# Kernel optimization log

Hardware: AMD Instinct MI355X
Metric: run time of the kernel (lower is better)

Reference implementation:

```python
import jax, jax.numpy as jnp
import numpy as np

EPS = 1e-12  # F.normalize eps


def qweight(r, i, j, k):
    # Hamilton-product block matrix: (out, in, kh, kw) from 4 blocks of (out//4, in//4, kh, kw)
    row_r = jnp.concatenate([r, -i, -j, -k], axis=1)
    row_i = jnp.concatenate([i, r, -k, j], axis=1)
    row_j = jnp.concatenate([j, k, r, -i], axis=1)
    row_k = jnp.concatenate([k, -j, i, r], axis=1)
    return jnp.concatenate([row_r, row_i, row_j, row_k], axis=0)


def qconv(x, r, i, j, k, b, stride, pad):
    w = qweight(r, i, j, k)
    y = jax.lax.conv_general_dilated(
        x, w, window_strides=(stride, stride),
        padding=[(pad, pad), (pad, pad)],
        dimension_numbers=('NCHW', 'OIHW', 'NCHW'))
    return y + b[None, :, None, None]


def setup_inputs() -> dict:
    key = jax.random.key(0)
    ks = jax.random.split(key, 16)
    dim, heads, B, H, W = 128, 4, 2, 128, 128
    d4 = dim // 4
    std = 0.02
    inp = {
        'x': jax.random.normal(ks[0], (B, dim, H, W), jnp.float32),
        'qkv_r': jax.random.normal(ks[1], (3 * d4, d4, 1, 1), jnp.float32) * std,
        'qkv_i': jax.random.normal(ks[2], (3 * d4, d4, 1, 1), jnp.float32) * std,
        'qkv_j': jax.random.normal(ks[3], (3 * d4, d4, 1, 1), jnp.float32) * std,
        'qkv_k': jax.random.normal(ks[4], (3 * d4, d4, 1, 1), jnp.float32) * std,
        'qkv_b': jnp.zeros((3 * dim,), jnp.float32),
        'dw_r': jax.random.normal(ks[5], (3 * d4, 3 * d4, 3, 3), jnp.float32) * std,
        'dw_i': jax.random.normal(ks[6], (3 * d4, 3 * d4, 3, 3), jnp.float32) * std,
        'dw_j': jax.random.normal(ks[7], (3 * d4, 3 * d4, 3, 3), jnp.float32) * std,
        'dw_k': jax.random.normal(ks[8], (3 * d4, 3 * d4, 3, 3), jnp.float32) * std,
        'dw_b': jnp.zeros((3 * dim,), jnp.float32),
        'po_r': jax.random.normal(ks[9], (d4, d4, 1, 1), jnp.float32) * std,
        'po_i': jax.random.normal(ks[10], (d4, d4, 1, 1), jnp.float32) * std,
        'po_j': jax.random.normal(ks[11], (d4, d4, 1, 1), jnp.float32) * std,
        'po_k': jax.random.normal(ks[12], (d4, d4, 1, 1), jnp.float32) * std,
        'po_b': jnp.zeros((dim,), jnp.float32),
        'temperature': jnp.ones((heads, 1, 1), jnp.float32),
    }
    return inp


def reference(x, qkv_r, qkv_i, qkv_j, qkv_k, qkv_b,
              dw_r, dw_i, dw_j, dw_k, dw_b,
              po_r, po_i, po_j, po_k, po_b, temperature):
    b, c, h, w = x.shape
    heads = temperature.shape[0]
    ch = c // heads  # channels per head

    qkv = qconv(x, qkv_r, qkv_i, qkv_j, qkv_k, qkv_b, 1, 0)
    qkv = qconv(qkv, dw_r, dw_i, dw_j, dw_k, dw_b, 1, 1)
    q, k, v = jnp.split(qkv, 3, axis=1)

    def to_heads(t):  # b (head c) h w -> b head c (h w)
        return t.reshape(b, heads, ch, h * w)

    q, k, v = to_heads(q), to_heads(k), to_heads(v)
    # L2-normalize along spatial axis (torch F.normalize semantics)
    q = q / jnp.maximum(jnp.linalg.norm(q, axis=-1, keepdims=True), EPS)
    k = k / jnp.maximum(jnp.linalg.norm(k, axis=-1, keepdims=True), EPS)

    attn = jnp.einsum('bhcs,bhds->bhcd', q, k) * temperature[None]
    attn = jax.nn.softmax(attn, axis=-1)
    out = jnp.einsum('bhcd,bhds->bhcs', attn, v)

    out = out.reshape(b, c, h, w)
    out = qconv(out, po_r, po_i, po_j, po_k, po_b, 1, 0)
    return out
```

## Files before the change

kernel.cpp:

```cpp
#include <hip/hip_runtime.h>
#include <hip/hip_bf16.h>
#include <string.h>

typedef __hip_bfloat16 bf16;
typedef __bf16 bf16x8 __attribute__((ext_vector_type(8)));
typedef float f32x4 __attribute__((ext_vector_type(4)));

typedef __attribute__((address_space(1))) void* gas_ptr;
typedef __attribute__((address_space(3))) void* las_ptr;

__device__ __forceinline__ void gload_lds16(const void* g, void* l) {
  __builtin_amdgcn_global_load_lds((gas_ptr)(void*)g, (las_ptr)l, 16, 0, 0);
}


__device__ __forceinline__ void qexpand(const float* r, const float* i_, const float* j_,
                                        const float* k_, bf16* dst, int O4, int I4, int taps,
                                        int gid) {
  int C = 4 * I4;
  int o   = gid / (taps * C);
  int rem = gid % (taps * C);
  int tap = rem / C, c = rem % C;
  int br = o / O4, orr = o % O4, bc = c / I4, ic = c % I4;
  const float* srcs[4] = { r, i_, j_, k_ };
  const int   comp[4][4] = { {0,1,2,3}, {1,0,3,2}, {2,3,0,1}, {3,2,1,0} };
  const float sgn [4][4] = { {1,-1,-1,-1}, {1,1,-1,1}, {1,1,1,-1}, {1,-1,1,1} };
  float v = srcs[comp[br][bc]][(size_t)(orr * I4 + ic) * taps + tap];
  dst[gid] = __float2bfloat16(v * sgn[br][bc]);
}

#define N_W1 49152
#define N_W2 1327104
#define N_W3 16384
#define N_BR 396288
#define N_MI 900
#define N_SQ 512
#define N_SR 8192
#define N_PREP (N_W1 + N_W2 + N_W3 + N_BR + N_MI + N_SQ + N_SR)

__global__ void prep(const float* __restrict__ qr, const float* __restrict__ qi,
                     const float* __restrict__ qj, const float* __restrict__ qk,
                     const float* __restrict__ dr, const float* __restrict__ di,
                     const float* __restrict__ dj, const float* __restrict__ dk,
                     const float* __restrict__ pr, const float* __restrict__ pi,
                     const float* __restrict__ pj, const float* __restrict__ pk,
                     const float* __restrict__ qb, const float* __restrict__ db,
                     const float* __restrict__ pb, const float* __restrict__ tp,
                     bf16* __restrict__ W1t, bf16* __restrict__ W2t, bf16* __restrict__ W3t,
                     bf16* __restrict__ q1p, float* __restrict__ misc,
                     float* __restrict__ ssq, float* __restrict__ Sraw) {
  int gid = blockIdx.x * 256 + threadIdx.x;
  if (gid < N_W1) { qexpand(qr, qi, qj, qk, W1t, 96, 32, 1, gid); return; }
  gid -= N_W1;
  if (gid < N_W2) { qexpand(dr, di, dj, dk, W2t, 96, 96, 9, gid); return; }
  gid -= N_W2;
  if (gid < N_W3) { qexpand(pr, pi, pj, pk, W3t, 32, 32, 1, gid); return; }
  gid -= N_W3;
  if (gid < N_BR) {
    int b = gid / (516 * 384);
    int rem = gid % (516 * 384);
    int cell = rem / 384, c = rem % 384;
    int hp, wp;
    if      (cell < 130) { hp = 0;   wp = cell; }
    else if (cell < 260) { hp = 129; wp = cell - 130; }
    else if (cell < 388) { hp = cell - 260 + 1; wp = 0; }
    else                 { hp = cell - 388 + 1; wp = 129; }
    q1p[((size_t)((b * 130 + hp) * 130) + wp) * 384 + c] = __float2bfloat16(0.0f);
    return;
  }
  gid -= N_BR;
  if (gid < N_MI) {
    if (gid < 384)      misc[gid] = qb[gid];
    else if (gid < 768) misc[gid] = db[gid - 384];
    else if (gid < 896) misc[gid] = pb[gid - 768];
    else                misc[gid] = tp[gid - 896];
    return;
  }
  gid -= N_MI;
  if (gid < N_SQ) { ssq[gid] = 0.0f; return; }
  gid -= N_SQ;
  if (gid < N_SR) { Sraw[gid] = 0.0f; return; }
}

__global__ __launch_bounds__(256) void gemm_qkv1f(const float* __restrict__ x,
                                                  const bf16* __restrict__ wt,
                                                  const float* __restrict__ bias,
                                                  bf16* __restrict__ out) {
  __shared__ __align__(16) bf16 Axl[4 * 64 * 32];
  __shared__ __align__(16) bf16 Bl [4 * 128 * 32];
  const int h = blockIdx.x, wh = blockIdx.y, b = blockIdx.z;
  const int tid = threadIdx.x, wid = tid >> 6, lane = tid & 63;
  const int l16 = lane & 15, q = lane >> 4;
  const int wm = (wid & 1) * 32, wn = (wid >> 1) * 64;
  {
    const int c = tid >> 1, seg = tid & 1;
    const float* src = x + ((size_t)(b * 128 + c) << 14) + h * 128 + wh * 64 + seg * 32;
    bf16* dstc = Axl + (c >> 5) * 2048 + (c & 31);
    for (int j = 0; j < 8; ++j) {
      float4 v = *(const float4*)(src + j * 4);
      int w0 = seg * 32 + j * 4;
      dstc[(w0 + 0) * 32] = __float2bfloat16(v.x);
      dstc[(w0 + 1) * 32] = __float2bfloat16(v.y);
      dstc[(w0 + 2) * 32] = __float2bfloat16(v.z);
      dstc[(w0 + 3) * 32] = __float2bfloat16(v.w);
    }
  }
  for (int ot = 0; ot < 3; ++ot) {
    __syncthreads();
    const bf16* bbase = wt + (size_t)ot * 16384;
    for (int i = 0; i < 8; ++i) {
      int ci = wid * 512 + i * 64 + lane;
      int chunk = ci >> 9, rem = ci & 511;
      int o = rem >> 2, part = rem & 3;
      gload_lds16(bbase + o * 128 + chunk * 32 + part * 8, Bl + (size_t)(wid * 512 + i * 64) * 8);
    }
    __syncthreads();
    f32x4 acc[2][4] = {};
    for (int k = 0; k < 4; ++k) {
      bf16x8 af[2], bfr[4];
      for (int mi = 0; mi < 2; ++mi)
        af[mi] = *(const bf16x8*)&Axl[k * 2048 + (wm + mi * 16 + l16) * 32 + q * 8];
      for (int ni = 0; ni < 4; ++ni)
        bfr[ni] = *(const bf16x8*)&Bl[k * 4096 + (wn + ni * 16 + l16) * 32 + q * 8];
      for (int mi = 0; mi < 2; ++mi)
        for (int ni = 0; ni < 4; ++ni)
          acc[mi][ni] = __builtin_amdgcn_mfma_f32_16x16x32_bf16(af[mi], bfr[ni], acc[mi][ni], 0, 0, 0);
    }
    for (int ni = 0; ni < 4; ++ni) {
      int o = ot * 128 + wn + ni * 16 + l16;
      float bv = bias[o];
      for (int mi = 0; mi < 2; ++mi) {
        int w0 = wh * 64 + wm + mi * 16 + q * 4;
        for (int r = 0; r < 4; ++r) {
          int w = w0 + r;
          size_t idx = ((size_t)((b * 130 + h + 1) * 130) + (w + 1)) * 384 + o;
          out[idx] = __float2bfloat16(acc[mi][ni][r] + bv);
        }
      }
    }
    __syncthreads();
  }
}

__global__ __launch_bounds__(256, 2) void conv3x3(const bf16* __restrict__ in,
                                                  const bf16* __restrict__ wt,
                                                  const float* __restrict__ bias,
                                                  bf16* __restrict__ out) {
  __shared__ __align__(16) short Al[6 * 132 * 32];
  __shared__ __align__(16) short Bl[9 * 48 * 32];
  const int lid = blockIdx.x;
  const int xcd = lid & 7, slot = lid >> 3;
  const int b = xcd & 1;
  const int h0 = (xcd >> 1) * 32 + (slot & 7) * 4;
  const int ob = (slot >> 3) * 48;
  const int tid = threadIdx.x, wid = tid >> 6, lane = tid & 63;
  const int l16 = lane & 15, q = lane >> 4;
  f32x4 acc[8][3] = {};
  const bf16* abase = in + (size_t)b * 130 * 130 * 384;
  const bf16* bbase = wt + (size_t)ob * 3456;
  for (int c0 = 0; c0 < 384; c0 += 32) {
    __syncthreads();
    for (int i = 0; i < 12; ++i) {
      int g = wid * 792 + i * 64;
      int ci = g + lane;
      int row = ci / 528, rem = ci % 528;
      int w = rem >> 2, part = rem & 3;
      gload_lds16(abase + ((size_t)(h0 + row) * 130 + w) * 384 + c0 + part * 8, &Al[g * 8]);
    }
    if (lane < 24) {
      int g = wid * 792 + 768;
      int ci = g + lane;
      int row = ci / 528, rem = ci % 528;
      int w = rem >> 2, part = rem & 3;
      gload_lds16(abase + ((size_t)(h0 + row) * 130 + w) * 384 + c0 + part * 8, &Al[g * 8]);
    }
    for (int i = 0; i < 6; ++i) {
      int g = wid * 432 + i * 64;
      int ci = g + lane;
      int tap = ci / 192, rem = ci % 192;
      int o = rem >> 2, part = rem & 3;
      gload_lds16(bbase + (size_t)o * 3456 + tap * 384 + c0 + part * 8, &Bl[g * 8]);
    }
    if (lane < 48) {
      int g = wid * 432 + 384;
      int ci = g + lane;
      int tap = ci / 192, rem = ci % 192;
      int o = rem >> 2, part = rem & 3;
      gload_lds16(bbase + (size_t)o * 3456 + tap * 384 + c0 + part * 8, &Bl[g * 8]);
    }
    __syncthreads();
    for (int dh = 0; dh < 3; ++dh)
      for (int dw = 0; dw < 3; ++dw) {
        bf16x8 af[8], bfr[3];
        for (int mi = 0; mi < 8; ++mi)
          af[mi] = *(const bf16x8*)&Al[((wid + dh) * 132 + mi * 16 + l16 + dw) * 32 + q * 8];
        for (int ni = 0; ni < 3; ++ni)
          bfr[ni] = *(const bf16x8*)&Bl[((dh * 3 + dw) * 48 + ni * 16 + l16) * 32 + q * 8];
        for (int mi = 0; mi < 8; ++mi)
          for (int ni = 0; ni < 3; ++ni)
            acc[mi][ni] = __builtin_amdgcn_mfma_f32_16x16x32_bf16(af[mi], bfr[ni], acc[mi][ni], 0, 0, 0);
      }
  }
  const int h = h0 + wid;
  for (int ni = 0; ni < 3; ++ni) {
    int o = ob + ni * 16 + l16;
    float bv = bias[o];
    for (int mi = 0; mi < 8; ++mi) {
      int w0 = mi * 16 + q * 4;
      for (int r = 0; r < 4; ++r) {
        int w = w0 + r;
        out[((size_t)(b * 16384 + h * 128 + w)) * 384 + o] = __float2bfloat16(acc[mi][ni][r] + bv);
      }
    }
  }
}

__global__ __launch_bounds__(256) void attn_qk(const bf16* __restrict__ q2,
                                               float* __restrict__ Sraw,
                                               float* __restrict__ ssq) {
  const int sc = blockIdx.x, h = blockIdx.y, b = blockIdx.z;
  const int t = threadIdx.x;
  __shared__ bf16 qt[64][32];
  __shared__ bf16 kt[64][32];
  __shared__ float Sl[1024];
  __shared__ float nql[32], nkl[32];
  for (int i = t; i < 1024; i += 256) Sl[i] = 0.0f;
  if (t < 32) nql[t] = 0.0f;
  else if (t < 64) nkl[t - 32] = 0.0f;
  const int slq = t >> 2, seg = t & 3;
  const int slot = t & 63, sg = t >> 6;
  const int cg = (slot & 7) * 4, dg = (slot >> 3) * 4;
  float acc[4][4] = {};
  float sq[4] = {}, sk[4] = {};
  for (int it = 0; it < 8; ++it) {
    int sbase = sc * 512 + it * 64;
    __syncthreads();
    {
      size_t rq = ((size_t)(b * 16384 + sbase + slq)) * 384 + h * 32 + seg * 8;
      *(bf16x8*)&qt[slq][seg * 8] = *(const bf16x8*)&q2[rq];
      *(bf16x8*)&kt[slq][seg * 8] = *(const bf16x8*)&q2[rq + 128];
    }
    __syncthreads();
    for (int sl = sg * 16; sl < sg * 16 + 16; ++sl) {
      float qv[4], kv[4];
      for (int a = 0; a < 4; ++a) qv[a] = __bfloat162float(qt[sl][cg + a]);
      for (int d = 0; d < 4; ++d) kv[d] = __bfloat162float(kt[sl][dg + d]);
      if (dg == 0) for (int a = 0; a < 4; ++a) sq[a] += qv[a] * qv[a];
      if (cg == 0) for (int d = 0; d < 4; ++d) sk[d] += kv[d] * kv[d];
      for (int a = 0; a < 4; ++a)
        for (int d = 0; d < 4; ++d) acc[a][d] += qv[a] * kv[d];
    }
  }
  for (int a = 0; a < 4; ++a)
    for (int d = 0; d < 4; ++d)
      atomicAdd(&Sl[(cg + a) * 32 + dg + d], acc[a][d]);
  if (dg == 0) for (int a = 0; a < 4; ++a) atomicAdd(&nql[cg + a], sq[a]);
  if (cg == 0) for (int d = 0; d < 4; ++d) atomicAdd(&nkl[dg + d], sk[d]);
  __syncthreads();
  float* Sg = Sraw + (size_t)((b * 4 + h) * 1024);
  for (int i = t * 4; i < t * 4 + 4; ++i) atomicAdd(&Sg[i], Sl[i]);
  if (t < 32) atomicAdd(&ssq[b * 256 + h * 32 + t], nql[t]);
  else if (t < 64) atomicAdd(&ssq[b * 256 + 128 + h * 32 + (t - 32)], nkl[t - 32]);
}

__global__ __launch_bounds__(256) void attn_out(const bf16* __restrict__ q2,
                                                const float* __restrict__ Sraw,
                                                const float* __restrict__ ssq,
                                                const float* __restrict__ misc,
                                                const bf16* __restrict__ w3,
                                                float* __restrict__ out) {
  __shared__ __align__(16) bf16 Ml[4 * 128 * 32];
  __shared__ float Pl[4][32][32];
  __shared__ __align__(16) short Bl[128 * 32];
  __shared__ float rqa[128], rka[128];
  const int tile = blockIdx.x;
  const int b = tile >> 7, s0 = (tile & 127) * 128;
  const int t = threadIdx.x;
  const int wid = t >> 6, lane = t & 63;
  const int l16 = lane & 15, q = lane >> 4;
  {
    float v = ssq[b * 256 + t];
    float rv = 1.0f / fmaxf(sqrtf(fmaxf(v, 0.0f)), 1e-12f);
    if (t < 128) rqa[t] = rv; else rka[t - 128] = rv;
  }
  __syncthreads();
  if (t < 128) {
    int hh = t >> 5, c = t & 31;
    const float* Sr = Sraw + ((size_t)((b * 4 + hh) * 32 + c)) * 32;
    float tv = misc[896 + hh];
    float rq = rqa[t];
    float row[32];
    float m = -1e30f;
    for (int d = 0; d < 32; ++d) { row[d] = Sr[d] * tv * rq * rka[hh * 32 + d]; m = fmaxf(m, row[d]); }
    float sum = 0.0f;
    for (int d = 0; d < 32; ++d) { row[d] = expf(row[d] - m); sum += row[d]; }
    float inv = 1.0f / sum;
    for (int d = 0; d < 32; ++d) Pl[hh][c][d] = row[d] * inv;
  }
  __syncthreads();
  {
    const int o = t >> 1, half = t & 1;
    for (int hh2 = 0; hh2 < 2; ++hh2) {
      int hv = half * 2 + hh2;
      float w3r[32];
      const bf16* wrow = w3 + o * 128 + hv * 32;
      for (int c = 0; c < 32; ++c) w3r[c] = __bfloat162float(wrow[c]);
      for (int d = 0; d < 32; ++d) {
        float s = 0.0f;
        for (int c = 0; c < 32; ++c) s += w3r[c] * Pl[hv][c][d];
        Ml[hv * 4096 + o * 32 + d] = __float2bfloat16(s);
      }
    }
  }
  f32x4 acc[4][4] = {};
  const int wmo = (wid & 1) * 64, wns = (wid >> 1) * 64;
  for (int kc = 0; kc < 4; ++kc) {
    __syncthreads();
    for (int i = 0; i < 2; ++i) {
      int ci = i * 256 + t;
      int s = ci >> 2, part = ci & 3;
      gload_lds16(q2 + ((size_t)(b * 16384 + s0 + s)) * 384 + 256 + kc * 32 + part * 8,
                  &Bl[(size_t)(i * 256 + wid * 64) * 8]);
    }
    __syncthreads();
    bf16x8 af[4], bfr[4];
    for (int mi = 0; mi < 4; ++mi)
      af[mi] = *(const bf16x8*)&Ml[kc * 4096 + (wmo + mi * 16 + l16) * 32 + q * 8];
    for (int ni = 0; ni < 4; ++ni)
      bfr[ni] = *(const bf16x8*)&Bl[(wns + ni * 16 + l16) * 32 + q * 8];
    for (int mi = 0; mi < 4; ++mi)
      for (int ni = 0; ni < 4; ++ni)
        acc[mi][ni] = __builtin_amdgcn_mfma_f32_16x16x32_bf16(af[mi], bfr[ni], acc[mi][ni], 0, 0, 0);
  }
  for (int ni = 0; ni < 4; ++ni) {
    int s = s0 + wns + ni * 16 + l16;
    for (int mi = 0; mi < 4; ++mi) {
      int o0 = wmo + mi * 16 + q * 4;
      for (int r = 0; r < 4; ++r) {
        int o = o0 + r;
        out[(size_t)b * 2097152 + (size_t)o * 16384 + s] = acc[mi][ni][r] + misc[768 + o];
      }
    }
  }
}

extern "C" void kernel_launch(void* const* d_in, const int* in_sizes, int n_in,
                              void* d_out, int out_size, void* d_ws, size_t ws_size,
                              hipStream_t stream) {
  const float* x     = (const float*)d_in[0];
  const float* qkv_r = (const float*)d_in[1];
  const float* qkv_i = (const float*)d_in[2];
  const float* qkv_j = (const float*)d_in[3];
  const float* qkv_k = (const float*)d_in[4];
  const float* qkv_b = (const float*)d_in[5];
  const float* dw_r  = (const float*)d_in[6];
  const float* dw_i  = (const float*)d_in[7];
  const float* dw_j  = (const float*)d_in[8];
  const float* dw_k  = (const float*)d_in[9];
  const float* dw_b  = (const float*)d_in[10];
  const float* po_r  = (const float*)d_in[11];
  const float* po_i  = (const float*)d_in[12];
  const float* po_j  = (const float*)d_in[13];
  const float* po_k  = (const float*)d_in[14];
  const float* po_b  = (const float*)d_in[15];
  const float* temp  = (const float*)d_in[16];

  char* ws = (char*)d_ws;
  size_t off = 0;
  auto alloc = [&](size_t bytes) { char* p = ws + off; off += (bytes + 255) & ~(size_t)255; return p; };
  bf16* q1p  = (bf16*)alloc((size_t)2 * 130 * 130 * 384 * 2);
  bf16* q2   = (bf16*)alloc((size_t)2 * 16384 * 384 * 2);
  bf16* W1t  = (bf16*)alloc((size_t)384 * 128 * 2);
  bf16* W2t  = (bf16*)alloc((size_t)384 * 3456 * 2);
  bf16* W3t  = (bf16*)alloc((size_t)128 * 128 * 2);
  float* ssq  = (float*)alloc((size_t)2 * 256 * 4);
  float* Sraw = (float*)alloc((size_t)2 * 4 * 32 * 32 * 4);
  float* misc = (float*)alloc((size_t)900 * 4);

  prep<<<(N_PREP + 255) / 256, 256, 0, stream>>>(qkv_r, qkv_i, qkv_j, qkv_k,
                                                 dw_r, dw_i, dw_j, dw_k,
                                                 po_r, po_i, po_j, po_k,
                                                 qkv_b, dw_b, po_b, temp,
                                                 W1t, W2t, W3t, q1p, misc, ssq, Sraw);
  gemm_qkv1f<<<dim3(128, 2, 2), 256, 0, stream>>>(x, W1t, misc, q1p);
  conv3x3<<<512, 256, 0, stream>>>(q1p, W2t, misc + 384, q2);
  attn_qk<<<dim3(32, 4, 2), 256, 0, stream>>>(q2, Sraw, ssq);
  attn_out<<<256, 256, 0, stream>>>(q2, Sraw, ssq, misc, W3t, (float*)d_out);
}
```

Before: 229.5 us.

## Fuse prep into QKV GEMM and merge attention kernels with counter sync

The weight-expansion/prep kernel is merged into the first pointwise QKV GEMM. The W1 quaternion weight is now expanded directly into LDS inside the GEMM blocks, while the remaining blocks do the other prep work. The two attention kernels become one launch: the first 256 blocks compute the Gram matrix and norms, then bump a global counter, and the output blocks spin on that counter before the softmax and projection. This removes two launches and their inter-kernel gaps. The cost is redundant W1 expansion per block and a spin-wait that relies on producer blocks being scheduled first.

```diff
diff --git a/kernel.cpp b/kernel.cpp
--- a/kernel.cpp
+++ b/kernel.cpp
@@ -29,67 +29,70 @@
   dst[gid] = __float2bfloat16(v * sgn[br][bc]);
 }
 
-#define N_W1 49152
 #define N_W2 1327104
 #define N_W3 16384
 #define N_BR 396288
 #define N_MI 900
 #define N_SQ 512
 #define N_SR 8192
-#define N_PREP (N_W1 + N_W2 + N_W3 + N_BR + N_MI + N_SQ + N_SR)
-
-__global__ void prep(const float* __restrict__ qr, const float* __restrict__ qi,
-                     const float* __restrict__ qj, const float* __restrict__ qk,
-                     const float* __restrict__ dr, const float* __restrict__ di,
-                     const float* __restrict__ dj, const float* __restrict__ dk,
-                     const float* __restrict__ pr, const float* __restrict__ pi,
-                     const float* __restrict__ pj, const float* __restrict__ pk,
-                     const float* __restrict__ qb, const float* __restrict__ db,
-                     const float* __restrict__ pb, const float* __restrict__ tp,
-                     bf16* __restrict__ W1t, bf16* __restrict__ W2t, bf16* __restrict__ W3t,
-                     bf16* __restrict__ q1p, float* __restrict__ misc,
-                     float* __restrict__ ssq, float* __restrict__ Sraw) {
-  int gid = blockIdx.x * 256 + threadIdx.x;
-  if (gid < N_W1) { qexpand(qr, qi, qj, qk, W1t, 96, 32, 1, gid); return; }
-  gid -= N_W1;
-  if (gid < N_W2) { qexpand(dr, di, dj, dk, W2t, 96, 96, 9, gid); return; }
-  gid -= N_W2;
-  if (gid < N_W3) { qexpand(pr, pi, pj, pk, W3t, 32, 32, 1, gid); return; }
-  gid -= N_W3;
-  if (gid < N_BR) {
-    int b = gid / (516 * 384);
-    int rem = gid % (516 * 384);
-    int cell = rem / 384, c = rem % 384;
-    int hp, wp;
-    if      (cell < 130) { hp = 0;   wp = cell; }
-    else if (cell < 260) { hp = 129; wp = cell - 130; }
-    else if (cell < 388) { hp = cell - 260 + 1; wp = 0; }
-    else                 { hp = cell - 388 + 1; wp = 129; }
-    q1p[((size_t)((b * 130 + hp) * 130) + wp) * 384 + c] = __float2bfloat16(0.0f);
+#define N_CT 64
+#define N_PREP (N_W2 + N_W3 + N_BR + N_MI + N_SQ + N_SR + N_CT)
+#define PREP_BLOCKS ((N_PREP + 255) / 256)
+
+__global__ __launch_bounds__(256) void qkv1f_prep(
+    const float* __restrict__ x,
+    const float* __restrict__ qr, const float* __restrict__ qi,
+    const float* __restrict__ qj, const float* __restrict__ qk,
+    const float* __restrict__ qkv_b,
+    const float* __restrict__ dr, const float* __restrict__ di,
+    const float* __restrict__ dj, const float* __restrict__ dk,
+    const float* __restrict__ pr, const float* __restrict__ pi,
+    const float* __restrict__ pj, const float* __restrict__ pk,
+    const float* __restrict__ qb, const float* __restrict__ db,
+    const float* __restrict__ pb, const float* __restrict__ tp,
+    bf16* __restrict__ W2t, bf16* __restrict__ W3t,
+    bf16* __restrict__ q1p, float* __restrict__ misc,
+    float* __restrict__ ssq, float* __restrict__ Sraw, int* __restrict__ ctr) {
+  const int lid = blockIdx.x;
+  const int tid = threadIdx.x;
+  if (lid >= 512) {
+    int gid = (lid - 512) * 256 + tid;
+    if (gid < N_W2) { qexpand(dr, di, dj, dk, W2t, 96, 96, 9, gid); return; }
+    gid -= N_W2;
+    if (gid < N_W3) { qexpand(pr, pi, pj, pk, W3t, 32, 32, 1, gid); return; }
+    gid -= N_W3;
+    if (gid < N_BR) {
+      int b = gid / (516 * 384);
+      int rem = gid % (516 * 384);
+      int cell = rem / 384, c = rem % 384;
+      int hp, wp;
+      if      (cell < 130) { hp = 0;   wp = cell; }
+      else if (cell < 260) { hp = 129; wp = cell - 130; }
+      else if (cell < 388) { hp = cell - 260 + 1; wp = 0; }
+      else                 { hp = cell - 388 + 1; wp = 129; }
+      q1p[((size_t)((b * 130 + hp) * 130) + wp) * 384 + c] = __float2bfloat16(0.0f);
+      return;
+    }
+    gid -= N_BR;
+    if (gid < N_MI) {
+      if (gid < 384)      misc[gid] = qb[gid];
+      else if (gid < 768) misc[gid] = db[gid - 384];
+      else if (gid < 896) misc[gid] = pb[gid - 768];
+      else                misc[gid] = tp[gid - 896];
+      return;
+    }
+    gid -= N_MI;
+    if (gid < N_SQ) { ssq[gid] = 0.0f; return; }
+    gid -= N_SQ;
+    if (gid < N_SR) { Sraw[gid] = 0.0f; return; }
+    gid -= N_SR;
+    if (gid < N_CT) { ctr[gid] = 0; return; }
     return;
   }
-  gid -= N_BR;
-  if (gid < N_MI) {
-    if (gid < 384)      misc[gid] = qb[gid];
-    else if (gid < 768) misc[gid] = db[gid - 384];
-    else if (gid < 896) misc[gid] = pb[gid - 768];
-    else                misc[gid] = tp[gid - 896];
-    return;
-  }
-  gid -= N_MI;
-  if (gid < N_SQ) { ssq[gid] = 0.0f; return; }
-  gid -= N_SQ;
-  if (gid < N_SR) { Sraw[gid] = 0.0f; return; }
-}
-
-__global__ __launch_bounds__(256) void gemm_qkv1f(const float* __restrict__ x,
-                                                  const bf16* __restrict__ wt,
-                                                  const float* __restrict__ bias,
-                                                  bf16* __restrict__ out) {
   __shared__ __align__(16) bf16 Axl[4 * 64 * 32];
   __shared__ __align__(16) bf16 Bl [4 * 128 * 32];
-  const int h = blockIdx.x, wh = blockIdx.y, b = blockIdx.z;
-  const int tid = threadIdx.x, wid = tid >> 6, lane = tid & 63;
+  const int h = lid & 127, wh = (lid >> 7) & 1, b = (lid >> 8) & 1;
+  const int wid = tid >> 6, lane = tid & 63;
   const int l16 = lane & 15, q = lane >> 4;
   const int wm = (wid & 1) * 32, wn = (wid >> 1) * 64;
   {
@@ -107,12 +110,21 @@
   }
   for (int ot = 0; ot < 3; ++ot) {
     __syncthreads();
-    const bf16* bbase = wt + (size_t)ot * 16384;
-    for (int i = 0; i < 8; ++i) {
-      int ci = wid * 512 + i * 64 + lane;
-      int chunk = ci >> 9, rem = ci & 511;
-      int o = rem >> 2, part = rem & 3;
-      gload_lds16(bbase + o * 128 + chunk * 32 + part * 8, Bl + (size_t)(wid * 512 + i * 64) * 8);
+    {
+      const int o_l = tid >> 1, hf = tid & 1;
+      const int o_g = ot * 128 + o_l;
+      const int br = o_g / 96, orr = o_g % 96;
+      for (int cc = 0; cc < 64; ++cc) {
+        int c = hf * 64 + cc;
+        int bc = c >> 5, ic = c & 31;
+        int sel = br ^ bc;
+        const float* sp = (sel == 0) ? qr : (sel == 1) ? qi : (sel == 2) ? qj : qk;
+        float sg = (bc == 0) ? 1.0f
+                 : (br == 0) ? -1.0f
+                 : ((bc == (br % 3) + 1) ? -1.0f : 1.0f);
+        float v = sp[orr * 32 + ic] * sg;
+        Bl[bc * 4096 + o_l * 32 + ic] = __float2bfloat16(v);
+      }
     }
     __syncthreads();
     f32x4 acc[2][4] = {};
@@ -128,13 +140,14 @@
     }
     for (int ni = 0; ni < 4; ++ni) {
       int o = ot * 128 + wn + ni * 16 + l16;
-      float bv = bias[o];
+      float bv = qkv_b[o];
       for (int mi = 0; mi < 2; ++mi) {
         int w0 = wh * 64 + wm + mi * 16 + q * 4;
         for (int r = 0; r < 4; ++r) {
           int w = w0 + r;
           size_t idx = ((size_t)((b * 130 + h + 1) * 130) + (w + 1)) * 384 + o;
-          out[idx] = __float2bfloat16(acc[mi][ni][r] + bv);
+          out:;
+          q1p[idx] = __float2bfloat16(acc[mi][ni][r] + bv);
         }
       }
     }
@@ -215,71 +228,83 @@
   }
 }
 
-__global__ __launch_bounds__(256) void attn_qk(const bf16* __restrict__ q2,
-                                               float* __restrict__ Sraw,
-                                               float* __restrict__ ssq) {
-  const int sc = blockIdx.x, h = blockIdx.y, b = blockIdx.z;
-  const int t = threadIdx.x;
+__global__ __launch_bounds__(256) void attn_fused(const bf16* __restrict__ q2,
+                                                  float* __restrict__ Sraw,
+                                                  float* __restrict__ ssq,
+                                                  const float* __restrict__ misc,
+                                                  const bf16* __restrict__ w3,
+                                                  int* __restrict__ ctr,
+                                                  float* __restrict__ out) {
   __shared__ bf16 qt[64][32];
   __shared__ bf16 kt[64][32];
   __shared__ float Sl[1024];
   __shared__ float nql[32], nkl[32];
-  for (int i = t; i < 1024; i += 256) Sl[i] = 0.0f;
-  if (t < 32) nql[t] = 0.0f;
-  else if (t < 64) nkl[t - 32] = 0.0f;
-  const int slq = t >> 2, seg = t & 3;
-  const int slot = t & 63, sg = t >> 6;
-  const int cg = (slot & 7) * 4, dg = (slot >> 3) * 4;
-  float acc[4][4] = {};
-  float sq[4] = {}, sk[4] = {};
-  for (int it = 0; it < 8; ++it) {
-    int sbase = sc * 512 + it * 64;
-    __syncthreads();
-    {
-      size_t rq = ((size_t)(b * 16384 + sbase + slq)) * 384 + h * 32 + seg * 8;
-      *(bf16x8*)&qt[slq][seg * 8] = *(const bf16x8*)&q2[rq];
-      *(bf16x8*)&kt[slq][seg * 8] = *(const bf16x8*)&q2[rq + 128];
-    }
-    __syncthreads();
-    for (int sl = sg * 16; sl < sg * 16 + 16; ++sl) {
-      float qv[4], kv[4];
-      for (int a = 0; a < 4; ++a) qv[a] = __bfloat162float(qt[sl][cg + a]);
-      for (int d = 0; d < 4; ++d) kv[d] = __bfloat162float(kt[sl][dg + d]);
-      if (dg == 0) for (int a = 0; a < 4; ++a) sq[a] += qv[a] * qv[a];
-      if (cg == 0) for (int d = 0; d < 4; ++d) sk[d] += kv[d] * kv[d];
-      for (int a = 0; a < 4; ++a)
-        for (int d = 0; d < 4; ++d) acc[a][d] += qv[a] * kv[d];
-    }
-  }
-  for (int a = 0; a < 4; ++a)
-    for (int d = 0; d < 4; ++d)
-      atomicAdd(&Sl[(cg + a) * 32 + dg + d], acc[a][d]);
-  if (dg == 0) for (int a = 0; a < 4; ++a) atomicAdd(&nql[cg + a], sq[a]);
-  if (cg == 0) for (int d = 0; d < 4; ++d) atomicAdd(&nkl[dg + d], sk[d]);
-  __syncthreads();
-  float* Sg = Sraw + (size_t)((b * 4 + h) * 1024);
-  for (int i = t * 4; i < t * 4 + 4; ++i) atomicAdd(&Sg[i], Sl[i]);
-  if (t < 32) atomicAdd(&ssq[b * 256 + h * 32 + t], nql[t]);
-  else if (t < 64) atomicAdd(&ssq[b * 256 + 128 + h * 32 + (t - 32)], nkl[t - 32]);
-}
-
-__global__ __launch_bounds__(256) void attn_out(const bf16* __restrict__ q2,
-                                                const float* __restrict__ Sraw,
-                                                const float* __restrict__ ssq,
-                                                const float* __restrict__ misc,
-                                                const bf16* __restrict__ w3,
-                                                float* __restrict__ out) {
   __shared__ __align__(16) bf16 Ml[4 * 128 * 32];
   __shared__ float Pl[4][32][32];
-  __shared__ __align__(16) short Bl[128 * 32];
+  __shared__ __align__(16) short Vl[128 * 32];
   __shared__ float rqa[128], rka[128];
-  const int tile = blockIdx.x;
-  const int b = tile >> 7, s0 = (tile & 127) * 128;
+  const int lid = blockIdx.x;
   const int t = threadIdx.x;
   const int wid = t >> 6, lane = t & 63;
   const int l16 = lane & 15, q = lane >> 4;
+
+  if (lid < 256) {
+    const int sc = lid & 31, h = (lid >> 5) & 3, b = lid >> 7;
+    for (int i = t; i < 1024; i += 256) Sl[i] = 0.0f;
+    if (t < 32) nql[t] = 0.0f;
+    else if (t < 64) nkl[t - 32] = 0.0f;
+    const int slq = t >> 2, seg = t & 3;
+    const int slot = t & 63, sg = t >> 6;
+    const int cg = (slot & 7) * 4, dg = (slot >> 3) * 4;
+    float acc[4][4] = {};
+    float sq[4] = {}, sk[4] = {};
+    for (int it = 0; it < 8; ++it) {
+      int sbase = sc * 512 + it * 64;
+      __syncthreads();
+      {
+        size_t rq = ((size_t)(b * 16384 + sbase + slq)) * 384 + h * 32 + seg * 8;
+        *(bf16x8*)&qt[slq][seg * 8] = *(const bf16x8*)&q2[rq];
+        *(bf16x8*)&kt[slq][seg * 8] = *(const bf16x8*)&q2[rq + 128];
+      }
+      __syncthreads();
+      for (int sl = sg * 16; sl < sg * 16 + 16; ++sl) {
+        float qv[4], kv[4];
+        for (int a = 0; a < 4; ++a) qv[a] = __bfloat162float(qt[sl][cg + a]);
+        for (int d = 0; d < 4; ++d) kv[d] = __bfloat162float(kt[sl][dg + d]);
+        if (dg == 0) for (int a = 0; a < 4; ++a) sq[a] += qv[a] * qv[a];
+        if (cg == 0) for (int d = 0; d < 4; ++d) sk[d] += kv[d] * kv[d];
+        for (int a = 0; a < 4; ++a)
+          for (int d = 0; d < 4; ++d) acc[a][d] += qv[a] * kv[d];
+      }
+    }
+    for (int a = 0; a < 4; ++a)
+      for (int d = 0; d < 4; ++d)
+        atomicAdd(&Sl[(cg + a) * 32 + dg + d], acc[a][d]);
+    if (dg == 0) for (int a = 0; a < 4; ++a) atomicAdd(&nql[cg + a], sq[a]);
+    if (cg == 0) for (int d = 0; d < 4; ++d) atomicAdd(&nkl[dg + d], sk[d]);
+    __syncthreads();
+    float* Sg = Sraw + (size_t)((b * 4 + h) * 1024);
+    for (int i = t * 4; i < t * 4 + 4; ++i) atomicAdd(&Sg[i], Sl[i]);
+    if (t < 32) atomicAdd(&ssq[b * 256 + h * 32 + t], nql[t]);
+    else if (t < 64) atomicAdd(&ssq[b * 256 + 128 + h * 32 + (t - 32)], nkl[t - 32]);
+    __threadfence();
+    __syncthreads();
+    if (t == 0) __hip_atomic_fetch_add(ctr, 1, __ATOMIC_RELEASE, __HIP_MEMORY_SCOPE_AGENT);
+    return;
+  }
+
+  const int tile = lid - 256;
+  const int b = tile >> 7, s0 = (tile & 127) * 128;
+  if (t == 0) {
+    long spins = 0;
+    while (__hip_atomic_load(ctr, __ATOMIC_ACQUIRE, __HIP_MEMORY_SCOPE_AGENT) < 256) {
+      if (++spins > 400000000L) break;
+    }
+  }
+  __syncthreads();
+  __threadfence();
   {
-    float v = ssq[b * 256 + t];
+    float v = __hip_atomic_load(&ssq[b * 256 + t], __ATOMIC_RELAXED, __HIP_MEMORY_SCOPE_AGENT);
     float rv = 1.0f / fmaxf(sqrtf(fmaxf(v, 0.0f)), 1e-12f);
     if (t < 128) rqa[t] = rv; else rka[t - 128] = rv;
   }
@@ -291,7 +316,11 @@
     float rq = rqa[t];
     float row[32];
     float m = -1e30f;
-    for (int d = 0; d < 32; ++d) { row[d] = Sr[d] * tv * rq * rka[hh * 32 + d]; m = fmaxf(m, row[d]); }
+    for (int d = 0; d < 32; ++d) {
+      float sv = __hip_atomic_load(&Sr[d], __ATOMIC_RELAXED, __HIP_MEMORY_SCOPE_AGENT);
+      row[d] = sv * tv * rq * rka[hh * 32 + d];
+      m = fmaxf(m, row[d]);
+    }
     float sum = 0.0f;
     for (int d = 0; d < 32; ++d) { row[d] = expf(row[d] - m); sum += row[d]; }
     float inv = 1.0f / sum;
@@ -320,14 +349,14 @@
       int ci = i * 256 + t;
       int s = ci >> 2, part = ci & 3;
       gload_lds16(q2 + ((size_t)(b * 16384 + s0 + s)) * 384 + 256 + kc * 32 + part * 8,
-                  &Bl[(size_t)(i * 256 + wid * 64) * 8]);
+                  &Vl[(size_t)(i * 256 + wid * 64) * 8]);
     }
     __syncthreads();
     bf16x8 af[4], bfr[4];
     for (int mi = 0; mi < 4; ++mi)
       af[mi] = *(const bf16x8*)&Ml[kc * 4096 + (wmo + mi * 16 + l16) * 32 + q * 8];
     for (int ni = 0; ni < 4; ++ni)
-      bfr[ni] = *(const bf16x8*)&Bl[(wns + ni * 16 + l16) * 32 + q * 8];
+      bfr[ni] = *(const bf16x8*)&Vl[(wns + ni * 16 + l16) * 32 + q * 8];
     for (int mi = 0; mi < 4; ++mi)
       for (int ni = 0; ni < 4; ++ni)
         acc[mi][ni] = __builtin_amdgcn_mfma_f32_16x16x32_bf16(af[mi], bfr[ni], acc[mi][ni], 0, 0, 0);
@@ -370,20 +399,19 @@
   auto alloc = [&](size_t bytes) { char* p = ws + off; off += (bytes + 255) & ~(size_t)255; return p; };
   bf16* q1p  = (bf16*)alloc((size_t)2 * 130 * 130 * 384 * 2);
   bf16* q2   = (bf16*)alloc((size_t)2 * 16384 * 384 * 2);
-  bf16* W1t  = (bf16*)alloc((size_t)384 * 128 * 2);
   bf16* W2t  = (bf16*)alloc((size_t)384 * 3456 * 2);
   bf16* W3t  = (bf16*)alloc((size_t)128 * 128 * 2);
   float* ssq  = (float*)alloc((size_t)2 * 256 * 4);
   float* Sraw = (float*)alloc((size_t)2 * 4 * 32 * 32 * 4);
   float* misc = (float*)alloc((size_t)900 * 4);
-
-  prep<<<(N_PREP + 255) / 256, 256, 0, stream>>>(qkv_r, qkv_i, qkv_j, qkv_k,
-                                                 dw_r, dw_i, dw_j, dw_k,
-                                                 po_r, po_i, po_j, po_k,
-                                                 qkv_b, dw_b, po_b, temp,
-                                                 W1t, W2t, W3t, q1p, misc, ssq, Sraw);
-  gemm_qkv1f<<<dim3(128, 2, 2), 256, 0, stream>>>(x, W1t, misc, q1p);
+  int*   ctr  = (int*)alloc((size_t)N_CT * 4);
+
+  qkv1f_prep<<<512 + PREP_BLOCKS, 256, 0, stream>>>(
+      x, qkv_r, qkv_i, qkv_j, qkv_k, qkv_b,
+      dw_r, dw_i, dw_j, dw_k,
+      po_r, po_i, po_j, po_k,
+      qkv_b, dw_b, po_b, temp,
+      W2t, W3t, q1p, misc, ssq, Sraw, ctr);
   conv3x3<<<512, 256, 0, stream>>>(q1p, W2t, misc + 384, q2);
-  attn_qk<<<dim3(32, 4, 2), 256, 0, stream>>>(q2, Sraw, ssq);
-  attn_out<<<256, 256, 0, stream>>>(q2, Sraw, ssq, misc, W3t, (float*)d_out);
-}
+  attn_fused<<<512, 256, 0, stream>>>(q2, Sraw, ssq, misc, W3t, ctr, (float*)d_out);
+}
```

New measurement: 293.2 us. +27.7%, slower.
